# Kernel optimization log

Measured on AMD Instinct MI355X. Metric: run time of the kernel, lower is better.

Reference implementation:

```python
import jax, jax.numpy as jnp
import numpy as np
from jax import lax

B, N = 8, 4096
NPOINT, RADIUS, NSAMPLE = 1024, 0.2, 32
MLP = [64, 64, 128]
FEAT = 64
ALPHA = 0.2          # LeakyReLU slope
BN_EPS = 1e-5        # BatchNorm eps (eval mode, running_mean=0, running_var=1)
BIG = 1e10


def setup_inputs() -> dict:
    key = jax.random.key(0)
    ks = jax.random.split(key, 16)
    xyz = jax.random.uniform(ks[0], (B, N, 3), dtype=jnp.float32)
    feats = jax.random.normal(ks[1], (B, N, FEAT), dtype=jnp.float32)
    d = {"points": jnp.concatenate([xyz, feats], axis=-1)}
    ch = [FEAT] + MLP
    for i in range(len(MLP)):
        d[f"W{i}"] = jax.random.normal(ks[2 + 3 * i], (ch[i + 1], ch[i]), dtype=jnp.float32) * 0.1
        d[f"b{i}"] = jnp.zeros((ch[i + 1],), jnp.float32)
        d[f"g{i}"] = jnp.ones((ch[i + 1],), jnp.float32)
        d[f"be{i}"] = jnp.zeros((ch[i + 1],), jnp.float32)
    d["a_att"] = jax.random.uniform(ks[12], (3 + MLP[-1], MLP[-1]), jnp.float32, -0.3, 0.3)
    return d


def _gather(points, idx):
    # points: [B, N, D], idx: [B, ...] -> [B, ..., D]
    return jax.vmap(lambda p, i: p[i])(points, idx)


def farthest_point_sample(xyz, npoint):
    # xyz: [B, N, 3] -> [B, npoint] (deterministic start at index 0)
    b, n, _ = xyz.shape
    def step(carry, _):
        distance, farthest = carry
        centered = jnp.take_along_axis(xyz, farthest[:, None, None], axis=1)  # [B,1,3]
        dist = jnp.sum((xyz - centered) ** 2, axis=-1)                        # [B,N]
        distance = jnp.minimum(distance, dist)
        return (distance, jnp.argmax(distance, axis=-1)), farthest
    init = (jnp.full((b, n), BIG, dtype=xyz.dtype), jnp.zeros((b,), dtype=jnp.int32))
    _, idxs = lax.scan(step, init, None, length=npoint)
    return jnp.transpose(idxs)  # [B, npoint]


def query_ball_point(nsample, radius, xyz, centered_xyz):
    # squared distances [B, npoint, N]
    d = (-2.0 * jnp.einsum('bpc,bnc->bpn', centered_xyz, xyz)
         + jnp.sum(centered_xyz ** 2, -1)[..., None]
         + jnp.sum(xyz ** 2, -1)[:, None, :])
    d = jnp.where(d > radius ** 2, BIG, d)
    order = jnp.argsort(d, axis=-1)[..., :nsample]                    # [B,np,ns]
    sv = jnp.take_along_axis(d, order, axis=-1)                       # sorted values
    first = order[..., 0:1]
    return jnp.where(sv == BIG, first, order)


def _mlp(x, params):
    # x: [..., C]; 1x1 conv + BN(eval, mean=0, var=1) + relu per layer
    for (W, b, g, be) in params:
        x = jnp.einsum('...c,oc->...o', x, W) + b
        x = x * (g / jnp.sqrt(1.0 + BN_EPS)) + be
        x = jax.nn.relu(x)
    return x


def reference(points, W0, b0, g0, be0, W1, b1, g1, be1, W2, b2, g2, be2, a_att):
    xyz = points[..., :3]
    feats = points[..., 3:]
    cidx = farthest_point_sample(xyz, NPOINT)          # [B, npoint]
    cxyz = _gather(xyz, cidx)                          # [B, npoint, 3]
    cfeat = _gather(feats, cidx)                       # [B, npoint, D]
    gidx = query_ball_point(NSAMPLE, RADIUS, xyz, cxyz)  # [B, npoint, nsample]
    gxyz = _gather(xyz, gidx)                          # [B, npoint, ns, 3]
    gfeat = _gather(feats, gidx)                       # [B, npoint, ns, D]

    params = [(W0, b0, g0, be0), (W1, b1, g1, be1), (W2, b2, g2, be2)]
    cfeat = _mlp(cfeat, params)                        # [B, npoint, D']
    gfeat = _mlp(gfeat, params)                        # [B, npoint, ns, D']

    cpts = jnp.concatenate([cxyz, cfeat], axis=-1)     # [B, npoint, 3+D']
    gpts = jnp.concatenate([gxyz, gfeat], axis=-1)     # [B, npoint, ns, 3+D']

    delta = gpts - cpts[:, :, None, :]
    att = jax.nn.leaky_relu(jnp.einsum('bpnc,cd->bpnd', delta, a_att), ALPHA)
    att = jax.nn.softmax(att, axis=2)                  # over nsample (eval: no dropout)
    gac = jnp.sum(att * gfeat, axis=2)                 # [B, npoint, D']
    return jnp.concatenate([cxyz, gac], axis=-1)       # [B, npoint, 3+D']
```

## Files before the change

### kernel.cpp

```cpp
#include <hip/hip_runtime.h>
#include <math.h>

#define NBATCH 8
#define NPTS 4096
#define NPOINT 1024
#define NSAMPLE 32
#define PTDIM 67
#define BIGF 1e10f

#define DPP_QUAD_XOR1 0xB1
#define DPP_QUAD_XOR2 0x4E
#define DPP_ROW_HALF_MIRROR 0x141
#define DPP_ROW_MIRROR 0x140
#define DPP_ROW_BCAST15 0x142
#define DPP_ROW_BCAST31 0x143

template <int CTRL>
__device__ inline float dpp_mov_f(float v) {
  int i = __float_as_int(v);
  return __int_as_float(__builtin_amdgcn_update_dpp(i, i, CTRL, 0xf, 0xf, false));
}
template <int CTRL>
__device__ inline unsigned dpp_mov_u(unsigned v) {
  return (unsigned)__builtin_amdgcn_update_dpp((int)v, (int)v, CTRL, 0xf, 0xf, false);
}
template <int CTRL>
__device__ inline void dpp_min2(unsigned& hi, unsigned& lo) {
  unsigned nh = dpp_mov_u<CTRL>(hi);
  unsigned nl = dpp_mov_u<CTRL>(lo);
  bool take = (nh < hi) || (nh == hi && nl < lo);
  hi = take ? nh : hi;
  lo = take ? nl : lo;
}
__device__ inline unsigned fmap(float d) {
  unsigned b = __float_as_uint(d);
  return ((int)b < 0) ? ~b : (b | 0x80000000u);
}
#define FMAP_INF 0xFF800000u

__device__ inline float red32_max(float v) {
  v = fmaxf(v, dpp_mov_f<DPP_QUAD_XOR1>(v));
  v = fmaxf(v, dpp_mov_f<DPP_QUAD_XOR2>(v));
  v = fmaxf(v, dpp_mov_f<DPP_ROW_HALF_MIRROR>(v));
  v = fmaxf(v, dpp_mov_f<DPP_ROW_MIRROR>(v));
  v = fmaxf(v, __shfl_xor(v, 16));
  return v;
}
__device__ inline float red32_sum(float v) {
  v += dpp_mov_f<DPP_QUAD_XOR1>(v);
  v += dpp_mov_f<DPP_QUAD_XOR2>(v);
  v += dpp_mov_f<DPP_ROW_HALF_MIRROR>(v);
  v += dpp_mov_f<DPP_ROW_MIRROR>(v);
  v += __shfl_xor(v, 16);
  return v;
}

struct FpsS {
  unsigned long long slots[2][4];
  int cidxS[NPOINT];
  float4 C[NPTS];
};
struct ProjS {
  float As[131 * 128];
  float w0[64 * 64], w1[64 * 64], w2[128 * 64];
  float bb0[64], ss0[64], ee0[64];
  float bb1[64], ss1[64], ee1[64];
  float bb2[128], ss2[128], ee2[128];
};
#define F1_SMEM (sizeof(ProjS) > sizeof(FpsS) ? sizeof(ProjS) : sizeof(FpsS))

__device__ void fps_body(char* smemRaw, const float* __restrict__ pts,
                         int* __restrict__ cidx, float* __restrict__ X,
                         float* __restrict__ Y, float* __restrict__ Z) {
#pragma clang fp contract(off)
  FpsS* S = (FpsS*)smemRaw;
  const int b = blockIdx.x, tid = threadIdx.x;
  const int w = tid >> 6, lane = tid & 63;
  const float* pb = pts + (size_t)b * NPTS * PTDIM;
  float2 px2[8], py2[8], pz2[8];
  float dl[16];
  #pragma unroll
  for (int k = 0; k < 16; k++) {
    int j = tid + (k << 8);
    const float* pj = pb + (size_t)j * PTDIM;
    float x = pj[0], y = pj[1], z = pj[2];
    if (k & 1) { px2[k >> 1].y = x; py2[k >> 1].y = y; pz2[k >> 1].y = z; }
    else       { px2[k >> 1].x = x; py2[k >> 1].x = y; pz2[k >> 1].x = z; }
    S->C[j] = make_float4(x, y, z, 0.0f);
    X[b * NPTS + j] = x; Y[b * NPTS + j] = y; Z[b * NPTS + j] = z;
    dl[k] = BIGF;
  }
  __syncthreads();
  int f = 0;
  float4 c0 = S->C[0];
  float cx = c0.x, cy = c0.y, cz = c0.z;
  for (int t = 0; t < NPOINT; t++) {
    if (tid == 0) S->cidxS[t] = f;
    float2 c2x = make_float2(cx, cx);
    float2 c2y = make_float2(cy, cy);
    float2 c2z = make_float2(cz, cz);
    #pragma unroll
    for (int m = 0; m < 8; m++) {
      float2 dx = px2[m] - c2x;
      float2 dy = py2[m] - c2y;
      float2 dz = pz2[m] - c2z;
      float2 d = (dx * dx + dy * dy) + dz * dz;
      dl[2 * m]     = fminf(dl[2 * m],     d.x);
      dl[2 * m + 1] = fminf(dl[2 * m + 1], d.y);
    }
    float u0 = fmaxf(dl[0], dl[1]),  u1 = fmaxf(dl[2], dl[3]);
    float u2 = fmaxf(dl[4], dl[5]),  u3 = fmaxf(dl[6], dl[7]);
    float u4 = fmaxf(dl[8], dl[9]),  u5 = fmaxf(dl[10], dl[11]);
    float u6 = fmaxf(dl[12], dl[13]), u7 = fmaxf(dl[14], dl[15]);
    float v0 = fmaxf(u0, u1), v1 = fmaxf(u2, u3);
    float v2 = fmaxf(u4, u5), v3 = fmaxf(u6, u7);
    float bv = fmaxf(fmaxf(v0, v1), fmaxf(v2, v3));
    float m = bv;
    m = fmaxf(m, dpp_mov_f<DPP_QUAD_XOR1>(m));
    m = fmaxf(m, dpp_mov_f<DPP_QUAD_XOR2>(m));
    m = fmaxf(m, dpp_mov_f<DPP_ROW_HALF_MIRROR>(m));
    m = fmaxf(m, dpp_mov_f<DPP_ROW_MIRROR>(m));
    m = fmaxf(m, dpp_mov_f<DPP_ROW_BCAST15>(m));
    m = fmaxf(m, dpp_mov_f<DPP_ROW_BCAST31>(m));
    unsigned wmaxbits = (unsigned)__builtin_amdgcn_readlane(__float_as_int(m), 63);
    unsigned c_[16];
    #pragma unroll
    for (int k = 0; k < 16; k++)
      c_[k] = (__float_as_uint(dl[k]) == wmaxbits) ? (unsigned)(tid + (k << 8)) : 0xFFFFFFFFu;
    unsigned q0 = min(c_[0], c_[1]),  q1 = min(c_[2], c_[3]);
    unsigned q2 = min(c_[4], c_[5]),  q3 = min(c_[6], c_[7]);
    unsigned q4 = min(c_[8], c_[9]),  q5 = min(c_[10], c_[11]);
    unsigned q6 = min(c_[12], c_[13]), q7 = min(c_[14], c_[15]);
    unsigned r0 = min(q0, q1), r1 = min(q2, q3), r2 = min(q4, q5), r3 = min(q6, q7);
    unsigned cand = min(min(r0, r1), min(r2, r3));
    cand = min(cand, dpp_mov_u<DPP_QUAD_XOR1>(cand));
    cand = min(cand, dpp_mov_u<DPP_QUAD_XOR2>(cand));
    cand = min(cand, dpp_mov_u<DPP_ROW_HALF_MIRROR>(cand));
    cand = min(cand, dpp_mov_u<DPP_ROW_MIRROR>(cand));
    cand = min(cand, dpp_mov_u<DPP_ROW_BCAST15>(cand));
    cand = min(cand, dpp_mov_u<DPP_ROW_BCAST31>(cand));
    unsigned jmin = (unsigned)__builtin_amdgcn_readlane((int)cand, 63);
    if (lane == 0)
      S->slots[t & 1][w] = ((unsigned long long)wmaxbits << 32) |
                           (unsigned long long)(NPTS - 1 - jmin);
    __syncthreads();
    unsigned long long s0 = S->slots[t & 1][0], s1 = S->slots[t & 1][1];
    unsigned long long s2 = S->slots[t & 1][2], s3 = S->slots[t & 1][3];
    unsigned long long m0 = s0 > s1 ? s0 : s1;
    unsigned long long m1 = s2 > s3 ? s2 : s3;
    unsigned long long best = m0 > m1 ? m0 : m1;
    f = NPTS - 1 - (int)(best & 0xFFFFFFFFull);
    float4 cc = S->C[f];
    cx = cc.x; cy = cc.y; cz = cc.z;
  }
  __syncthreads();
  for (int i = tid; i < NPOINT; i += 256) cidx[b * NPOINT + i] = S->cidxS[i];
}

__device__ void projmlp_body(char* smemRaw, const float* __restrict__ pts,
    const float* __restrict__ W0, const float* __restrict__ B0, const float* __restrict__ G0, const float* __restrict__ E0,
    const float* __restrict__ W1, const float* __restrict__ B1, const float* __restrict__ G1, const float* __restrict__ E1,
    const float* __restrict__ W2, const float* __restrict__ B2, const float* __restrict__ G2, const float* __restrict__ E2,
    const float* __restrict__ Aatt,
    float* __restrict__ mfeat, float* __restrict__ P) {
  ProjS* S = (ProjS*)smemRaw;
  const float INVS = 0.99999500003750f;
  const int t = threadIdx.x;
  for (int i = t; i < 131 * 128; i += 256) S->As[i] = Aatt[i];
  for (int i = t; i < 4096; i += 256) { S->w0[i] = W0[i]; S->w1[i] = W1[i]; }
  for (int i = t; i < 8192; i += 256) S->w2[i] = W2[i];
  if (t < 64) {
    S->bb0[t] = B0[t]; S->ss0[t] = G0[t] * INVS; S->ee0[t] = E0[t];
    S->bb1[t] = B1[t]; S->ss1[t] = G1[t] * INVS; S->ee1[t] = E1[t];
  }
  if (t < 128) { S->bb2[t] = B2[t]; S->ss2[t] = G2[t] * INVS; S->ee2[t] = E2[t]; }
  __syncthreads();

  const int pb = blockIdx.x - 8;
  for (int rr = 0; rr < 2; rr++) {
    const size_t r = (size_t)pb * 512 + rr * 256 + t;
    const float* xr = pts + r * PTDIM + 3;
    float x[64];
    #pragma unroll
    for (int c = 0; c < 64; c++) x[c] = xr[c];

    float h1[64];
    #pragma unroll
    for (int o = 0; o < 64; o++) {
      float acc = S->bb0[o];
      #pragma unroll
      for (int c = 0; c < 64; c += 4) {
        float4 wv = *(const float4*)&S->w0[o * 64 + c];
        acc = fmaf(wv.x, x[c], acc);
        acc = fmaf(wv.y, x[c + 1], acc);
        acc = fmaf(wv.z, x[c + 2], acc);
        acc = fmaf(wv.w, x[c + 3], acc);
      }
      h1[o] = fmaxf(fmaf(acc, S->ss0[o], S->ee0[o]), 0.0f);
    }
    float h2[64];
    #pragma unroll
    for (int o = 0; o < 64; o++) {
      float acc = S->bb1[o];
      #pragma unroll
      for (int c = 0; c < 64; c += 4) {
        float4 wv = *(const float4*)&S->w1[o * 64 + c];
        acc = fmaf(wv.x, h1[c], acc);
        acc = fmaf(wv.y, h1[c + 1], acc);
        acc = fmaf(wv.z, h1[c + 2], acc);
        acc = fmaf(wv.w, h1[c + 3], acc);
      }
      h2[o] = fmaxf(fmaf(acc, S->ss1[o], S->ee1[o]), 0.0f);
    }
    float h3[128];
    float* orow = mfeat + r * 128;
    #pragma unroll
    for (int o = 0; o < 128; o += 4) {
      float a0 = S->bb2[o], a1 = S->bb2[o + 1], a2 = S->bb2[o + 2], a3 = S->bb2[o + 3];
      #pragma unroll
      for (int c = 0; c < 64; c += 4) {
        float4 wv0 = *(const float4*)&S->w2[(o    ) * 64 + c];
        float4 wv1 = *(const float4*)&S->w2[(o + 1) * 64 + c];
        float4 wv2 = *(const float4*)&S->w2[(o + 2) * 64 + c];
        float4 wv3 = *(const float4*)&S->w2[(o + 3) * 64 + c];
        a0 = fmaf(wv0.x, h2[c], a0); a0 = fmaf(wv0.y, h2[c+1], a0); a0 = fmaf(wv0.z, h2[c+2], a0); a0 = fmaf(wv0.w, h2[c+3], a0);
        a1 = fmaf(wv1.x, h2[c], a1); a1 = fmaf(wv1.y, h2[c+1], a1); a1 = fmaf(wv1.z, h2[c+2], a1); a1 = fmaf(wv1.w, h2[c+3], a1);
        a2 = fmaf(wv2.x, h2[c], a2); a2 = fmaf(wv2.y, h2[c+1], a2); a2 = fmaf(wv2.z, h2[c+2], a2); a2 = fmaf(wv2.w, h2[c+3], a2);
        a3 = fmaf(wv3.x, h2[c], a3); a3 = fmaf(wv3.y, h2[c+1], a3); a3 = fmaf(wv3.z, h2[c+2], a3); a3 = fmaf(wv3.w, h2[c+3], a3);
      }
      float4 ov;
      ov.x = fmaxf(fmaf(a0, S->ss2[o    ], S->ee2[o    ]), 0.0f);
      ov.y = fmaxf(fmaf(a1, S->ss2[o + 1], S->ee2[o + 1]), 0.0f);
      ov.z = fmaxf(fmaf(a2, S->ss2[o + 2], S->ee2[o + 2]), 0.0f);
      ov.w = fmaxf(fmaf(a3, S->ss2[o + 3], S->ee2[o + 3]), 0.0f);
      h3[o] = ov.x; h3[o + 1] = ov.y; h3[o + 2] = ov.z; h3[o + 3] = ov.w;
      *(float4*)(orow + o) = ov;
    }
    const float* pr = pts + r * PTDIM;
    float x0 = pr[0], y0 = pr[1], z0 = pr[2];
    float* prow = P + r * 128;
    for (int grp = 0; grp < 4; grp++) {
      const int g0 = grp * 32;
      float acc[32];
      #pragma unroll
      for (int j = 0; j < 32; j++) {
        float a0 = S->As[0 * 128 + g0 + j];
        float a1 = S->As[1 * 128 + g0 + j];
        float a2 = S->As[2 * 128 + g0 + j];
        acc[j] = fmaf(z0, a2, fmaf(y0, a1, x0 * a0));
      }
      #pragma unroll
      for (int c = 0; c < 128; c++) {
        float s = h3[c];
        const float* arow = &S->As[(3 + c) * 128 + g0];
        #pragma unroll
        for (int j = 0; j < 32; j += 4) {
          float4 a = *(const float4*)&arow[j];
          acc[j]   = fmaf(s, a.x, acc[j]);
          acc[j+1] = fmaf(s, a.y, acc[j+1]);
          acc[j+2] = fmaf(s, a.z, acc[j+2]);
          acc[j+3] = fmaf(s, a.w, acc[j+3]);
        }
      }
      #pragma unroll
      for (int j = 0; j < 32; j += 4)
        *(float4*)(prow + g0 + j) = make_float4(acc[j], acc[j+1], acc[j+2], acc[j+3]);
    }
  }
}

__global__ __launch_bounds__(256) void f1_kernel(const float* __restrict__ pts,
    const float* __restrict__ W0, const float* __restrict__ B0, const float* __restrict__ G0, const float* __restrict__ E0,
    const float* __restrict__ W1, const float* __restrict__ B1, const float* __restrict__ G1, const float* __restrict__ E1,
    const float* __restrict__ W2, const float* __restrict__ B2, const float* __restrict__ G2, const float* __restrict__ E2,
    const float* __restrict__ Aatt,
    float* __restrict__ mfeat, float* __restrict__ P, int* __restrict__ cidx,
    float* __restrict__ X, float* __restrict__ Y, float* __restrict__ Z) {
  __shared__ __align__(16) char smem[F1_SMEM];
  if (blockIdx.x < 8)
    fps_body(smem, pts, cidx, X, Y, Z);
  else
    projmlp_body(smem, pts, W0, B0, G0, E0, W1, B1, G1, E1, W2, B2, G2, E2,
                 Aatt, mfeat, P);
}

__global__ __launch_bounds__(256) void f2_kernel(
    const float* __restrict__ X, const float* __restrict__ Y, const float* __restrict__ Z,
    const int* __restrict__ cidx, int* __restrict__ gidx) {
  __shared__ float dbuf[4][512];
  __shared__ int   ibuf[4][512];
  const int t = threadIdx.x;
  const int w = t >> 6, lane = t & 63;
  const int pc = blockIdx.x * 4 + w;
  const int b = pc >> 10;
  const float* Xb = X + b * NPTS;
  const float* Yb = Y + b * NPTS;
  const float* Zb = Z + b * NPTS;
  const int cI = cidx[pc];
  const float cx = Xb[cI], cy = Yb[cI], cz = Zb[cI];
  const float sc = __fadd_rn(__fadd_rn(__fmul_rn(cx, cx), __fmul_rn(cy, cy)), __fmul_rn(cz, cz));
  const float R2 = 0.04f;
  int cnt = 0;
  for (int rr = 0; rr < 16; rr++) {
    const int base = rr * 256 + lane * 4;
    float4 px4 = *(const float4*)(Xb + base);
    float4 py4 = *(const float4*)(Yb + base);
    float4 pz4 = *(const float4*)(Zb + base);
    #pragma unroll
    for (int e = 0; e < 4; e++) {
      float px = e == 0 ? px4.x : e == 1 ? px4.y : e == 2 ? px4.z : px4.w;
      float py = e == 0 ? py4.x : e == 1 ? py4.y : e == 2 ? py4.z : py4.w;
      float pz = e == 0 ? pz4.x : e == 1 ? pz4.y : e == 2 ? pz4.z : pz4.w;
      float dot = __fadd_rn(__fadd_rn(__fmul_rn(cx, px), __fmul_rn(cy, py)), __fmul_rn(cz, pz));
      float sx  = __fadd_rn(__fadd_rn(__fmul_rn(px, px), __fmul_rn(py, py)), __fmul_rn(pz, pz));
      float d   = __fadd_rn(__fadd_rn(__fmul_rn(-2.0f, dot), sc), sx);
      bool pred = !(d > R2);
      unsigned long long mask = __ballot(pred);
      if (pred) {
        int pos = cnt + (int)__popcll(mask & ((1ull << lane) - 1ull));
        if (pos < 512) { dbuf[w][pos] = d; ibuf[w][pos] = base + e; }
      }
      cnt += (int)__popcll(mask);
    }
  }
  const int K = cnt < 512 ? cnt : 512;
  unsigned long long kk[8];
  #pragma unroll
  for (int k = 0; k < 8; k++) {
    int pos = lane + 64 * k;
    if (pos < K)
      kk[k] = ((unsigned long long)fmap(dbuf[w][pos]) << 32) | (unsigned)ibuf[w][pos];
    else
      kk[k] = ((unsigned long long)FMAP_INF << 32) | 0x7fffffffu;
  }
  int first = 0;
  int* gout = gidx + pc * NSAMPLE;
  for (int it = 0; it < NSAMPLE; it++) {
    unsigned long long best = kk[0];
    #pragma unroll
    for (int k = 1; k < 8; k++) if (kk[k] < best) best = kk[k];
    unsigned hi = (unsigned)(best >> 32), lo = (unsigned)best;
    dpp_min2<DPP_QUAD_XOR1>(hi, lo);
    dpp_min2<DPP_QUAD_XOR2>(hi, lo);
    dpp_min2<DPP_ROW_HALF_MIRROR>(hi, lo);
    dpp_min2<DPP_ROW_MIRROR>(hi, lo);
    dpp_min2<DPP_ROW_BCAST15>(hi, lo);
    dpp_min2<DPP_ROW_BCAST31>(hi, lo);
    unsigned blo = (unsigned)__builtin_amdgcn_readlane((int)lo, 63);
    #pragma unroll
    for (int k = 0; k < 8; k++)
      if ((unsigned)kk[k] == blo)
        kk[k] = (kk[k] & 0xFFFFFFFFull) | ((unsigned long long)FMAP_INF << 32);
    if (it == 0) first = (int)blo;
    if (lane == 0) gout[it] = (it < K) ? (int)blo : first;
  }
}

__global__ __launch_bounds__(256) void attn_kernel(
    const float* __restrict__ X, const float* __restrict__ Y, const float* __restrict__ Z,
    const float* __restrict__ mfeat, const float* __restrict__ P,
    const int* __restrict__ cidx, const int* __restrict__ gidx,
    float* __restrict__ out) {
  __shared__ float pcS[128];
  const int pc = (blockIdx.x & 7) * 1024 + (blockIdx.x >> 3);
  const int b = pc >> 10;
  const int t = threadIdx.x;
  const int n = t & 31, q = t >> 5;
  const int cI = cidx[pc];
  if (t < 128) pcS[t] = P[((size_t)b * NPTS + cI) * 128 + t];
  const int g = gidx[pc * NSAMPLE + n];
  const float* Pg = P + ((size_t)b * NPTS + g) * 128 + q * 16;
  const float* Gf = mfeat + ((size_t)b * NPTS + g) * 128 + q * 16;
  __syncthreads();
  float a[16], gfv[16];
  #pragma unroll
  for (int k = 0; k < 4; k++) {
    float4 vg = *(const float4*)(Pg + 4 * k);
    float4 vc = *(const float4*)&pcS[q * 16 + 4 * k];
    float4 vf = *(const float4*)(Gf + 4 * k);
    a[4*k]   = vg.x - vc.x; a[4*k+1] = vg.y - vc.y;
    a[4*k+2] = vg.z - vc.z; a[4*k+3] = vg.w - vc.w;
    gfv[4*k] = vf.x; gfv[4*k+1] = vf.y; gfv[4*k+2] = vf.z; gfv[4*k+3] = vf.w;
  }
  #pragma unroll
  for (int j = 0; j < 16; j++) a[j] = a[j] >= 0.0f ? a[j] : 0.2f * a[j];
  float e[16], s[16], num[16];
  #pragma unroll
  for (int j = 0; j < 16; j++) {
    float mx = red32_max(a[j]);
    e[j] = expf(a[j] - mx);
  }
  #pragma unroll
  for (int j = 0; j < 16; j++) s[j] = red32_sum(e[j]);
  #pragma unroll
  for (int j = 0; j < 16; j++) num[j] = red32_sum(e[j] * gfv[j]);
  if (n == 0) {
    float* orow = out + (size_t)pc * 131;
    #pragma unroll
    for (int j = 0; j < 16; j++) orow[3 + q * 16 + j] = num[j] / s[j];
    if (q == 0) {
      orow[0] = X[b * NPTS + cI]; orow[1] = Y[b * NPTS + cI]; orow[2] = Z[b * NPTS + cI];
    }
  }
}

extern "C" void kernel_launch(void* const* d_in, const int* in_sizes, int n_in,
                              void* d_out, int out_size, void* d_ws, size_t ws_size,
                              hipStream_t stream) {
  const float* points = (const float*)d_in[0];
  const float* W0 = (const float*)d_in[1];
  const float* B0 = (const float*)d_in[2];
  const float* G0 = (const float*)d_in[3];
  const float* E0 = (const float*)d_in[4];
  const float* W1 = (const float*)d_in[5];
  const float* B1 = (const float*)d_in[6];
  const float* G1 = (const float*)d_in[7];
  const float* E1 = (const float*)d_in[8];
  const float* W2 = (const float*)d_in[9];
  const float* B2 = (const float*)d_in[10];
  const float* G2 = (const float*)d_in[11];
  const float* E2 = (const float*)d_in[12];
  const float* Aatt = (const float*)d_in[13];
  float* out = (float*)d_out;

  float* mfeat = (float*)d_ws;
  float* Pw = mfeat + (size_t)NBATCH * NPTS * 128;
  float* Xw = Pw + (size_t)NBATCH * NPTS * 128;
  float* Yw = Xw + NBATCH * NPTS;
  float* Zw = Yw + NBATCH * NPTS;
  int* cidxw = (int*)(Zw + NBATCH * NPTS);
  int* gidxw = cidxw + NBATCH * NPOINT;

  f1_kernel<<<8 + 64, 256, 0, stream>>>(points,
      W0, B0, G0, E0, W1, B1, G1, E1, W2, B2, G2, E2, Aatt,
      mfeat, Pw, cidxw, Xw, Yw, Zw);
  f2_kernel<<<NBATCH * NPOINT / 4, 256, 0, stream>>>(Xw, Yw, Zw, cidxw, gidxw);
  attn_kernel<<<NBATCH * NPOINT, 256, 0, stream>>>(Xw, Yw, Zw, mfeat, Pw, cidxw, gidxw, out);
}
```

Measured before the change: 835.1 us.

## Carry winner coordinates through FPS argmax reduction instead of LDS lookup

The farthest-point-sampling loop now runs a single fused argmax reduction that carries the winning point's index and xyz coordinates through the in-register, DPP and cross-wave stages. This replaces the two-pass scheme (max value, then min index) and drops the shared-memory coordinate table and its dependent load after each barrier. It also skips the unused final distance update. The cost is more DPP moves and selects per reduction step (five values instead of one), in exchange for a shorter serial dependency chain per iteration.

```diff
diff --git a/kernel.cpp b/kernel.cpp
--- a/kernel.cpp
+++ b/kernel.cpp
@@ -55,10 +55,25 @@
   return v;
 }
 
+template <int CTRL>
+__device__ inline void dpp_amax(unsigned& hi, unsigned& lo,
+                                float& x, float& y, float& z) {
+  unsigned nh = dpp_mov_u<CTRL>(hi);
+  unsigned nl = dpp_mov_u<CTRL>(lo);
+  float nx = dpp_mov_f<CTRL>(x);
+  float ny = dpp_mov_f<CTRL>(y);
+  float nz = dpp_mov_f<CTRL>(z);
+  unsigned long long k  = ((unsigned long long)hi << 32) | lo;
+  unsigned long long nk = ((unsigned long long)nh << 32) | nl;
+  bool take = nk > k;
+  hi = take ? nh : hi; lo = take ? nl : lo;
+  x  = take ? nx : x;  y  = take ? ny : y;  z = take ? nz : z;
+}
+
 struct FpsS {
-  unsigned long long slots[2][4];
+  uint4 slotA[2][4];
+  float slotZ[2][4];
   int cidxS[NPOINT];
-  float4 C[NPTS];
 };
 struct ProjS {
   float As[131 * 128];
@@ -86,16 +101,15 @@
     float x = pj[0], y = pj[1], z = pj[2];
     if (k & 1) { px2[k >> 1].y = x; py2[k >> 1].y = y; pz2[k >> 1].y = z; }
     else       { px2[k >> 1].x = x; py2[k >> 1].x = y; pz2[k >> 1].x = z; }
-    S->C[j] = make_float4(x, y, z, 0.0f);
     X[b * NPTS + j] = x; Y[b * NPTS + j] = y; Z[b * NPTS + j] = z;
     dl[k] = BIGF;
   }
-  __syncthreads();
+  const unsigned jb = 4095u - (unsigned)tid;
   int f = 0;
-  float4 c0 = S->C[0];
-  float cx = c0.x, cy = c0.y, cz = c0.z;
+  float cx = pb[0], cy = pb[1], cz = pb[2];
   for (int t = 0; t < NPOINT; t++) {
     if (tid == 0) S->cidxS[t] = f;
+    if (t == NPOINT - 1) break;
     float2 c2x = make_float2(cx, cx);
     float2 c2y = make_float2(cy, cy);
     float2 c2z = make_float2(cz, cz);
@@ -108,50 +122,89 @@
       dl[2 * m]     = fminf(dl[2 * m],     d.x);
       dl[2 * m + 1] = fminf(dl[2 * m + 1], d.y);
     }
-    float u0 = fmaxf(dl[0], dl[1]),  u1 = fmaxf(dl[2], dl[3]);
-    float u2 = fmaxf(dl[4], dl[5]),  u3 = fmaxf(dl[6], dl[7]);
-    float u4 = fmaxf(dl[8], dl[9]),  u5 = fmaxf(dl[10], dl[11]);
-    float u6 = fmaxf(dl[12], dl[13]), u7 = fmaxf(dl[14], dl[15]);
-    float v0 = fmaxf(u0, u1), v1 = fmaxf(u2, u3);
-    float v2 = fmaxf(u4, u5), v3 = fmaxf(u6, u7);
-    float bv = fmaxf(fmaxf(v0, v1), fmaxf(v2, v3));
-    float m = bv;
-    m = fmaxf(m, dpp_mov_f<DPP_QUAD_XOR1>(m));
-    m = fmaxf(m, dpp_mov_f<DPP_QUAD_XOR2>(m));
-    m = fmaxf(m, dpp_mov_f<DPP_ROW_HALF_MIRROR>(m));
-    m = fmaxf(m, dpp_mov_f<DPP_ROW_MIRROR>(m));
-    m = fmaxf(m, dpp_mov_f<DPP_ROW_BCAST15>(m));
-    m = fmaxf(m, dpp_mov_f<DPP_ROW_BCAST31>(m));
-    unsigned wmaxbits = (unsigned)__builtin_amdgcn_readlane(__float_as_int(m), 63);
-    unsigned c_[16];
-    #pragma unroll
-    for (int k = 0; k < 16; k++)
-      c_[k] = (__float_as_uint(dl[k]) == wmaxbits) ? (unsigned)(tid + (k << 8)) : 0xFFFFFFFFu;
-    unsigned q0 = min(c_[0], c_[1]),  q1 = min(c_[2], c_[3]);
-    unsigned q2 = min(c_[4], c_[5]),  q3 = min(c_[6], c_[7]);
-    unsigned q4 = min(c_[8], c_[9]),  q5 = min(c_[10], c_[11]);
-    unsigned q6 = min(c_[12], c_[13]), q7 = min(c_[14], c_[15]);
-    unsigned r0 = min(q0, q1), r1 = min(q2, q3), r2 = min(q4, q5), r3 = min(q6, q7);
-    unsigned cand = min(min(r0, r1), min(r2, r3));
-    cand = min(cand, dpp_mov_u<DPP_QUAD_XOR1>(cand));
-    cand = min(cand, dpp_mov_u<DPP_QUAD_XOR2>(cand));
-    cand = min(cand, dpp_mov_u<DPP_ROW_HALF_MIRROR>(cand));
-    cand = min(cand, dpp_mov_u<DPP_ROW_MIRROR>(cand));
-    cand = min(cand, dpp_mov_u<DPP_ROW_BCAST15>(cand));
-    cand = min(cand, dpp_mov_u<DPP_ROW_BCAST31>(cand));
-    unsigned jmin = (unsigned)__builtin_amdgcn_readlane((int)cand, 63);
-    if (lane == 0)
-      S->slots[t & 1][w] = ((unsigned long long)wmaxbits << 32) |
-                           (unsigned long long)(NPTS - 1 - jmin);
+    float td[8]; unsigned tj[8]; float tx[8], ty[8], tz[8];
+    #pragma unroll
+    for (int m = 0; m < 8; m++) {
+      bool take = dl[2 * m + 1] > dl[2 * m];
+      td[m] = take ? dl[2 * m + 1] : dl[2 * m];
+      tj[m] = jb - (unsigned)((take ? (2 * m + 1) : (2 * m)) << 8);
+      tx[m] = take ? px2[m].y : px2[m].x;
+      ty[m] = take ? py2[m].y : py2[m].x;
+      tz[m] = take ? pz2[m].y : pz2[m].x;
+    }
+    #pragma unroll
+    for (int m = 0; m < 4; m++) {
+      bool take = td[2 * m + 1] > td[2 * m];
+      td[m] = take ? td[2 * m + 1] : td[2 * m];
+      tj[m] = take ? tj[2 * m + 1] : tj[2 * m];
+      tx[m] = take ? tx[2 * m + 1] : tx[2 * m];
+      ty[m] = take ? ty[2 * m + 1] : ty[2 * m];
+      tz[m] = take ? tz[2 * m + 1] : tz[2 * m];
+    }
+    #pragma unroll
+    for (int m = 0; m < 2; m++) {
+      bool take = td[2 * m + 1] > td[2 * m];
+      td[m] = take ? td[2 * m + 1] : td[2 * m];
+      tj[m] = take ? tj[2 * m + 1] : tj[2 * m];
+      tx[m] = take ? tx[2 * m + 1] : tx[2 * m];
+      ty[m] = take ? ty[2 * m + 1] : ty[2 * m];
+      tz[m] = take ? tz[2 * m + 1] : tz[2 * m];
+    }
+    {
+      bool take = td[1] > td[0];
+      td[0] = take ? td[1] : td[0];
+      tj[0] = take ? tj[1] : tj[0];
+      tx[0] = take ? tx[1] : tx[0];
+      ty[0] = take ? ty[1] : ty[0];
+      tz[0] = take ? tz[1] : tz[0];
+    }
+    unsigned bhi = __float_as_uint(td[0]);
+    unsigned bjp = tj[0];
+    float bx = tx[0], by = ty[0], bz = tz[0];
+    dpp_amax<DPP_QUAD_XOR1>(bhi, bjp, bx, by, bz);
+    dpp_amax<DPP_QUAD_XOR2>(bhi, bjp, bx, by, bz);
+    dpp_amax<DPP_ROW_HALF_MIRROR>(bhi, bjp, bx, by, bz);
+    dpp_amax<DPP_ROW_MIRROR>(bhi, bjp, bx, by, bz);
+    dpp_amax<DPP_ROW_BCAST15>(bhi, bjp, bx, by, bz);
+    dpp_amax<DPP_ROW_BCAST31>(bhi, bjp, bx, by, bz);
+    if (lane == 63) {
+      S->slotA[t & 1][w] = make_uint4(bhi, bjp, __float_as_uint(bx),
+                                      __float_as_uint(by));
+      S->slotZ[t & 1][w] = bz;
+    }
     __syncthreads();
-    unsigned long long s0 = S->slots[t & 1][0], s1 = S->slots[t & 1][1];
-    unsigned long long s2 = S->slots[t & 1][2], s3 = S->slots[t & 1][3];
-    unsigned long long m0 = s0 > s1 ? s0 : s1;
-    unsigned long long m1 = s2 > s3 ? s2 : s3;
-    unsigned long long best = m0 > m1 ? m0 : m1;
-    f = NPTS - 1 - (int)(best & 0xFFFFFFFFull);
-    float4 cc = S->C[f];
-    cx = cc.x; cy = cc.y; cz = cc.z;
+    uint4 q0 = S->slotA[t & 1][0]; float z0 = S->slotZ[t & 1][0];
+    uint4 q1 = S->slotA[t & 1][1]; float z1 = S->slotZ[t & 1][1];
+    uint4 q2 = S->slotA[t & 1][2]; float z2 = S->slotZ[t & 1][2];
+    uint4 q3 = S->slotA[t & 1][3]; float z3 = S->slotZ[t & 1][3];
+    {
+      unsigned long long k0 = ((unsigned long long)q0.x << 32) | q0.y;
+      unsigned long long k1 = ((unsigned long long)q1.x << 32) | q1.y;
+      bool take = k1 > k0;
+      q0.x = take ? q1.x : q0.x; q0.y = take ? q1.y : q0.y;
+      q0.z = take ? q1.z : q0.z; q0.w = take ? q1.w : q0.w;
+      z0   = take ? z1 : z0;
+    }
+    {
+      unsigned long long k2 = ((unsigned long long)q2.x << 32) | q2.y;
+      unsigned long long k3 = ((unsigned long long)q3.x << 32) | q3.y;
+      bool take = k3 > k2;
+      q2.x = take ? q3.x : q2.x; q2.y = take ? q3.y : q2.y;
+      q2.z = take ? q3.z : q2.z; q2.w = take ? q3.w : q2.w;
+      z2   = take ? z3 : z2;
+    }
+    {
+      unsigned long long k0 = ((unsigned long long)q0.x << 32) | q0.y;
+      unsigned long long k2 = ((unsigned long long)q2.x << 32) | q2.y;
+      bool take = k2 > k0;
+      q0.y = take ? q2.y : q0.y;
+      q0.z = take ? q2.z : q0.z; q0.w = take ? q2.w : q0.w;
+      z0   = take ? z2 : z0;
+    }
+    f = (int)(4095u - q0.y);
+    cx = __uint_as_float(q0.z);
+    cy = __uint_as_float(q0.w);
+    cz = z0;
   }
   __syncthreads();
   for (int i = tid; i < NPOINT; i += 256) cidx[b * NPOINT + i] = S->cidxS[i];
```

New measurement: 1.235 ms. +47.9%, slower.

## Fuse FPS, ball query and attention into one persistent producer-consumer kernel

Applied to the files above, without the earlier changes.

Merges the three launches into one kernel. FPS blocks publish each centroid index to global memory with an atomic store as soon as it is picked. Consumer blocks spin on those flags and immediately run the ball query and the attention softmax for each centroid, waiting on a per-batch done counter before reading the MLP projections. The goal is to hide the neighbour search and attention work behind the long serial FPS loop and to drop the gidx round trip and extra launches. In exchange it relies on every block being resident at the same time, on spin-waits with a capped retry count, and on only 128 consumer blocks handling all of the attention work.

```diff
diff --git a/kernel.cpp b/kernel.cpp
--- a/kernel.cpp
+++ b/kernel.cpp
@@ -7,6 +7,8 @@
 #define NSAMPLE 32
 #define PTDIM 67
 #define BIGF 1e10f
+#define NCONS 128
+#define SPIN_CAP 4096
 
 #define DPP_QUAD_XOR1 0xB1
 #define DPP_QUAD_XOR2 0x4E
@@ -57,7 +59,6 @@
 
 struct FpsS {
   unsigned long long slots[2][4];
-  int cidxS[NPOINT];
   float4 C[NPTS];
 };
 struct ProjS {
@@ -67,7 +68,15 @@
   float bb1[64], ss1[64], ee1[64];
   float bb2[128], ss2[128], ee2[128];
 };
-#define F1_SMEM (sizeof(ProjS) > sizeof(FpsS) ? sizeof(ProjS) : sizeof(FpsS))
+struct ConsS {
+  float dbuf[4][512];
+  int   ibuf[4][512];
+  int   gidxS[4][32];
+  int   cIS[4];
+  float pcS[128];
+};
+#define SMX1 (sizeof(ProjS) > sizeof(FpsS) ? sizeof(ProjS) : sizeof(FpsS))
+#define F1_SMEM (SMX1 > sizeof(ConsS) ? SMX1 : sizeof(ConsS))
 
 __device__ void fps_body(char* smemRaw, const float* __restrict__ pts,
                          int* __restrict__ cidx, float* __restrict__ X,
@@ -90,12 +99,15 @@
     X[b * NPTS + j] = x; Y[b * NPTS + j] = y; Z[b * NPTS + j] = z;
     dl[k] = BIGF;
   }
+  __threadfence();
   __syncthreads();
   int f = 0;
   float4 c0 = S->C[0];
   float cx = c0.x, cy = c0.y, cz = c0.z;
   for (int t = 0; t < NPOINT; t++) {
-    if (tid == 0) S->cidxS[t] = f;
+    if (tid == 0)
+      __hip_atomic_store(&cidx[b * NPOINT + t], f, __ATOMIC_RELAXED,
+                         __HIP_MEMORY_SCOPE_AGENT);
     float2 c2x = make_float2(cx, cx);
     float2 c2y = make_float2(cy, cy);
     float2 c2z = make_float2(cz, cz);
@@ -153,8 +165,6 @@
     float4 cc = S->C[f];
     cx = cc.x; cy = cc.y; cz = cc.z;
   }
-  __syncthreads();
-  for (int i = tid; i < NPOINT; i += 256) cidx[b * NPOINT + i] = S->cidxS[i];
 }
 
 __device__ void projmlp_body(char* smemRaw, const float* __restrict__ pts,
@@ -162,7 +172,7 @@
     const float* __restrict__ W1, const float* __restrict__ B1, const float* __restrict__ G1, const float* __restrict__ E1,
     const float* __restrict__ W2, const float* __restrict__ B2, const float* __restrict__ G2, const float* __restrict__ E2,
     const float* __restrict__ Aatt,
-    float* __restrict__ mfeat, float* __restrict__ P) {
+    float* __restrict__ mfeat, float* __restrict__ P, int* __restrict__ done) {
   ProjS* S = (ProjS*)smemRaw;
   const float INVS = 0.99999500003750f;
   const int t = threadIdx.x;
@@ -267,141 +277,170 @@
         *(float4*)(prow + g0 + j) = make_float4(acc[j], acc[j+1], acc[j+2], acc[j+3]);
     }
   }
-}
-
-__global__ __launch_bounds__(256) void f1_kernel(const float* __restrict__ pts,
+  __threadfence();
+  __syncthreads();
+  if (t == 0)
+    __hip_atomic_fetch_add(&done[pb >> 3], 1, __ATOMIC_RELEASE,
+                           __HIP_MEMORY_SCOPE_AGENT);
+}
+
+__device__ void consumer_body(char* smemRaw,
+    const float* __restrict__ X, const float* __restrict__ Y, const float* __restrict__ Z,
+    const float* __restrict__ mfeat, const float* __restrict__ P,
+    int* __restrict__ cidx, int* __restrict__ done,
+    float* __restrict__ out, int c) {
+  ConsS* S = (ConsS*)smemRaw;
+  const int t = threadIdx.x;
+  const int w = t >> 6, lane = t & 63;
+  const int b = c >> 4, r = c & 15;
+  const float* Xb = X + b * NPTS;
+  const float* Yb = Y + b * NPTS;
+  const float* Zb = Z + b * NPTS;
+  const float R2 = 0.04f;
+
+  for (int i = 0; i < 16; i++) {
+    const int tpos = r + 16 * (4 * i + w);
+    const int pc = b * NPOINT + tpos;
+    for (int spin = 0; spin < SPIN_CAP; ++spin) {
+      if (__hip_atomic_load(&cidx[pc], __ATOMIC_RELAXED,
+                            __HIP_MEMORY_SCOPE_AGENT) != -1) break;
+      __builtin_amdgcn_s_sleep(64);
+    }
+    int cI = __hip_atomic_load(&cidx[pc], __ATOMIC_ACQUIRE,
+                               __HIP_MEMORY_SCOPE_AGENT);
+    if (cI < 0) cI = 0;
+    if (lane == 0) S->cIS[w] = cI;
+    const float cx = Xb[cI], cy = Yb[cI], cz = Zb[cI];
+    const float sc = __fadd_rn(__fadd_rn(__fmul_rn(cx, cx), __fmul_rn(cy, cy)), __fmul_rn(cz, cz));
+    int cnt = 0;
+    for (int rr = 0; rr < 16; rr++) {
+      const int base = rr * 256 + lane * 4;
+      float4 px4 = *(const float4*)(Xb + base);
+      float4 py4 = *(const float4*)(Yb + base);
+      float4 pz4 = *(const float4*)(Zb + base);
+      #pragma unroll
+      for (int e = 0; e < 4; e++) {
+        float px = e == 0 ? px4.x : e == 1 ? px4.y : e == 2 ? px4.z : px4.w;
+        float py = e == 0 ? py4.x : e == 1 ? py4.y : e == 2 ? py4.z : py4.w;
+        float pz = e == 0 ? pz4.x : e == 1 ? pz4.y : e == 2 ? pz4.z : pz4.w;
+        float dot = __fadd_rn(__fadd_rn(__fmul_rn(cx, px), __fmul_rn(cy, py)), __fmul_rn(cz, pz));
+        float sx  = __fadd_rn(__fadd_rn(__fmul_rn(px, px), __fmul_rn(py, py)), __fmul_rn(pz, pz));
+        float d   = __fadd_rn(__fadd_rn(__fmul_rn(-2.0f, dot), sc), sx);
+        bool pred = !(d > R2);
+        unsigned long long mask = __ballot(pred);
+        if (pred) {
+          int pos = cnt + (int)__popcll(mask & ((1ull << lane) - 1ull));
+          if (pos < 512) { S->dbuf[w][pos] = d; S->ibuf[w][pos] = base + e; }
+        }
+        cnt += (int)__popcll(mask);
+      }
+    }
+    const int K = cnt < 512 ? cnt : 512;
+    unsigned long long kk[8];
+    #pragma unroll
+    for (int kq = 0; kq < 8; kq++) {
+      int pos = lane + 64 * kq;
+      if (pos < K)
+        kk[kq] = ((unsigned long long)fmap(S->dbuf[w][pos]) << 32) | (unsigned)S->ibuf[w][pos];
+      else
+        kk[kq] = ((unsigned long long)FMAP_INF << 32) | 0x7fffffffu;
+    }
+    int first = 0;
+    for (int it = 0; it < NSAMPLE; it++) {
+      unsigned long long best = kk[0];
+      #pragma unroll
+      for (int kq = 1; kq < 8; kq++) if (kk[kq] < best) best = kk[kq];
+      unsigned hi = (unsigned)(best >> 32), lo = (unsigned)best;
+      dpp_min2<DPP_QUAD_XOR1>(hi, lo);
+      dpp_min2<DPP_QUAD_XOR2>(hi, lo);
+      dpp_min2<DPP_ROW_HALF_MIRROR>(hi, lo);
+      dpp_min2<DPP_ROW_MIRROR>(hi, lo);
+      dpp_min2<DPP_ROW_BCAST15>(hi, lo);
+      dpp_min2<DPP_ROW_BCAST31>(hi, lo);
+      unsigned blo = (unsigned)__builtin_amdgcn_readlane((int)lo, 63);
+      #pragma unroll
+      for (int kq = 0; kq < 8; kq++)
+        if ((unsigned)kk[kq] == blo)
+          kk[kq] = (kk[kq] & 0xFFFFFFFFull) | ((unsigned long long)FMAP_INF << 32);
+      if (it == 0) first = (int)blo;
+      if (lane == 0) S->gidxS[w][it] = (it < K) ? (int)blo : first;
+    }
+    __syncthreads();
+    if (i == 0) {
+      for (int spin = 0; spin < SPIN_CAP; ++spin) {
+        if (__hip_atomic_load(&done[b], __ATOMIC_ACQUIRE,
+                              __HIP_MEMORY_SCOPE_AGENT) >= 8) break;
+        __builtin_amdgcn_s_sleep(64);
+      }
+    }
+    for (int cc = 0; cc < 4; cc++) {
+      const int pcc = b * NPOINT + r + 16 * (4 * i + cc);
+      const int cIc = S->cIS[cc];
+      if (t < 128) S->pcS[t] = P[((size_t)b * NPTS + cIc) * 128 + t];
+      __syncthreads();
+      const int n = t & 31, q = t >> 5;
+      const int g = S->gidxS[cc][n];
+      const float* Pg = P + ((size_t)b * NPTS + g) * 128 + q * 16;
+      const float* Gf = mfeat + ((size_t)b * NPTS + g) * 128 + q * 16;
+      float a[16], gfv[16];
+      #pragma unroll
+      for (int kq = 0; kq < 4; kq++) {
+        float4 vg = *(const float4*)(Pg + 4 * kq);
+        float4 vc = *(const float4*)&S->pcS[q * 16 + 4 * kq];
+        float4 vf = *(const float4*)(Gf + 4 * kq);
+        a[4*kq]   = vg.x - vc.x; a[4*kq+1] = vg.y - vc.y;
+        a[4*kq+2] = vg.z - vc.z; a[4*kq+3] = vg.w - vc.w;
+        gfv[4*kq] = vf.x; gfv[4*kq+1] = vf.y; gfv[4*kq+2] = vf.z; gfv[4*kq+3] = vf.w;
+      }
+      #pragma unroll
+      for (int j = 0; j < 16; j++) a[j] = a[j] >= 0.0f ? a[j] : 0.2f * a[j];
+      float e[16], s[16], num[16];
+      #pragma unroll
+      for (int j = 0; j < 16; j++) {
+        float mx = red32_max(a[j]);
+        e[j] = expf(a[j] - mx);
+      }
+      #pragma unroll
+      for (int j = 0; j < 16; j++) s[j] = red32_sum(e[j]);
+      #pragma unroll
+      for (int j = 0; j < 16; j++) num[j] = red32_sum(e[j] * gfv[j]);
+      if (n == 0) {
+        float* orow = out + (size_t)pcc * 131;
+        #pragma unroll
+        for (int j = 0; j < 16; j++) orow[3 + q * 16 + j] = num[j] / s[j];
+        if (q == 0) {
+          orow[0] = Xb[cIc]; orow[1] = Yb[cIc]; orow[2] = Zb[cIc];
+        }
+      }
+      __syncthreads();
+    }
+  }
+}
+
+__global__ __launch_bounds__(256) void mega_kernel(const float* __restrict__ pts,
     const float* __restrict__ W0, const float* __restrict__ B0, const float* __restrict__ G0, const float* __restrict__ E0,
     const float* __restrict__ W1, const float* __restrict__ B1, const float* __restrict__ G1, const float* __restrict__ E1,
     const float* __restrict__ W2, const float* __restrict__ B2, const float* __restrict__ G2, const float* __restrict__ E2,
     const float* __restrict__ Aatt,
     float* __restrict__ mfeat, float* __restrict__ P, int* __restrict__ cidx,
-    float* __restrict__ X, float* __restrict__ Y, float* __restrict__ Z) {
+    int* __restrict__ done,
+    float* __restrict__ X, float* __restrict__ Y, float* __restrict__ Z,
+    float* __restrict__ out) {
   __shared__ __align__(16) char smem[F1_SMEM];
   if (blockIdx.x < 8)
     fps_body(smem, pts, cidx, X, Y, Z);
+  else if (blockIdx.x < 72)
+    projmlp_body(smem, pts, W0, B0, G0, E0, W1, B1, G1, E1, W2, B2, G2, E2,
+                 Aatt, mfeat, P, done);
   else
-    projmlp_body(smem, pts, W0, B0, G0, E0, W1, B1, G1, E1, W2, B2, G2, E2,
-                 Aatt, mfeat, P);
-}
-
-__global__ __launch_bounds__(256) void f2_kernel(
-    const float* __restrict__ X, const float* __restrict__ Y, const float* __restrict__ Z,
-    const int* __restrict__ cidx, int* __restrict__ gidx) {
-  __shared__ float dbuf[4][512];
-  __shared__ int   ibuf[4][512];
-  const int t = threadIdx.x;
-  const int w = t >> 6, lane = t & 63;
-  const int pc = blockIdx.x * 4 + w;
-  const int b = pc >> 10;
-  const float* Xb = X + b * NPTS;
-  const float* Yb = Y + b * NPTS;
-  const float* Zb = Z + b * NPTS;
-  const int cI = cidx[pc];
-  const float cx = Xb[cI], cy = Yb[cI], cz = Zb[cI];
-  const float sc = __fadd_rn(__fadd_rn(__fmul_rn(cx, cx), __fmul_rn(cy, cy)), __fmul_rn(cz, cz));
-  const float R2 = 0.04f;
-  int cnt = 0;
-  for (int rr = 0; rr < 16; rr++) {
-    const int base = rr * 256 + lane * 4;
-    float4 px4 = *(const float4*)(Xb + base);
-    float4 py4 = *(const float4*)(Yb + base);
-    float4 pz4 = *(const float4*)(Zb + base);
-    #pragma unroll
-    for (int e = 0; e < 4; e++) {
-      float px = e == 0 ? px4.x : e == 1 ? px4.y : e == 2 ? px4.z : px4.w;
-      float py = e == 0 ? py4.x : e == 1 ? py4.y : e == 2 ? py4.z : py4.w;
-      float pz = e == 0 ? pz4.x : e == 1 ? pz4.y : e == 2 ? pz4.z : pz4.w;
-      float dot = __fadd_rn(__fadd_rn(__fmul_rn(cx, px), __fmul_rn(cy, py)), __fmul_rn(cz, pz));
-      float sx  = __fadd_rn(__fadd_rn(__fmul_rn(px, px), __fmul_rn(py, py)), __fmul_rn(pz, pz));
-      float d   = __fadd_rn(__fadd_rn(__fmul_rn(-2.0f, dot), sc), sx);
-      bool pred = !(d > R2);
-      unsigned long long mask = __ballot(pred);
-      if (pred) {
-        int pos = cnt + (int)__popcll(mask & ((1ull << lane) - 1ull));
-        if (pos < 512) { dbuf[w][pos] = d; ibuf[w][pos] = base + e; }
-      }
-      cnt += (int)__popcll(mask);
-    }
-  }
-  const int K = cnt < 512 ? cnt : 512;
-  unsigned long long kk[8];
-  #pragma unroll
-  for (int k = 0; k < 8; k++) {
-    int pos = lane + 64 * k;
-    if (pos < K)
-      kk[k] = ((unsigned long long)fmap(dbuf[w][pos]) << 32) | (unsigned)ibuf[w][pos];
-    else
-      kk[k] = ((unsigned long long)FMAP_INF << 32) | 0x7fffffffu;
-  }
-  int first = 0;
-  int* gout = gidx + pc * NSAMPLE;
-  for (int it = 0; it < NSAMPLE; it++) {
-    unsigned long long best = kk[0];
-    #pragma unroll
-    for (int k = 1; k < 8; k++) if (kk[k] < best) best = kk[k];
-    unsigned hi = (unsigned)(best >> 32), lo = (unsigned)best;
-    dpp_min2<DPP_QUAD_XOR1>(hi, lo);
-    dpp_min2<DPP_QUAD_XOR2>(hi, lo);
-    dpp_min2<DPP_ROW_HALF_MIRROR>(hi, lo);
-    dpp_min2<DPP_ROW_MIRROR>(hi, lo);
-    dpp_min2<DPP_ROW_BCAST15>(hi, lo);
-    dpp_min2<DPP_ROW_BCAST31>(hi, lo);
-    unsigned blo = (unsigned)__builtin_amdgcn_readlane((int)lo, 63);
-    #pragma unroll
-    for (int k = 0; k < 8; k++)
-      if ((unsigned)kk[k] == blo)
-        kk[k] = (kk[k] & 0xFFFFFFFFull) | ((unsigned long long)FMAP_INF << 32);
-    if (it == 0) first = (int)blo;
-    if (lane == 0) gout[it] = (it < K) ? (int)blo : first;
-  }
-}
-
-__global__ __launch_bounds__(256) void attn_kernel(
-    const float* __restrict__ X, const float* __restrict__ Y, const float* __restrict__ Z,
-    const float* __restrict__ mfeat, const float* __restrict__ P,
-    const int* __restrict__ cidx, const int* __restrict__ gidx,
-    float* __restrict__ out) {
-  __shared__ float pcS[128];
-  const int pc = (blockIdx.x & 7) * 1024 + (blockIdx.x >> 3);
-  const int b = pc >> 10;
-  const int t = threadIdx.x;
-  const int n = t & 31, q = t >> 5;
-  const int cI = cidx[pc];
-  if (t < 128) pcS[t] = P[((size_t)b * NPTS + cI) * 128 + t];
-  const int g = gidx[pc * NSAMPLE + n];
-  const float* Pg = P + ((size_t)b * NPTS + g) * 128 + q * 16;
-  const float* Gf = mfeat + ((size_t)b * NPTS + g) * 128 + q * 16;
-  __syncthreads();
-  float a[16], gfv[16];
-  #pragma unroll
-  for (int k = 0; k < 4; k++) {
-    float4 vg = *(const float4*)(Pg + 4 * k);
-    float4 vc = *(const float4*)&pcS[q * 16 + 4 * k];
-    float4 vf = *(const float4*)(Gf + 4 * k);
-    a[4*k]   = vg.x - vc.x; a[4*k+1] = vg.y - vc.y;
-    a[4*k+2] = vg.z - vc.z; a[4*k+3] = vg.w - vc.w;
-    gfv[4*k] = vf.x; gfv[4*k+1] = vf.y; gfv[4*k+2] = vf.z; gfv[4*k+3] = vf.w;
-  }
-  #pragma unroll
-  for (int j = 0; j < 16; j++) a[j] = a[j] >= 0.0f ? a[j] : 0.2f * a[j];
-  float e[16], s[16], num[16];
-  #pragma unroll
-  for (int j = 0; j < 16; j++) {
-    float mx = red32_max(a[j]);
-    e[j] = expf(a[j] - mx);
-  }
-  #pragma unroll
-  for (int j = 0; j < 16; j++) s[j] = red32_sum(e[j]);
-  #pragma unroll
-  for (int j = 0; j < 16; j++) num[j] = red32_sum(e[j] * gfv[j]);
-  if (n == 0) {
-    float* orow = out + (size_t)pc * 131;
-    #pragma unroll
-    for (int j = 0; j < 16; j++) orow[3 + q * 16 + j] = num[j] / s[j];
-    if (q == 0) {
-      orow[0] = X[b * NPTS + cI]; orow[1] = Y[b * NPTS + cI]; orow[2] = Z[b * NPTS + cI];
-    }
-  }
+    consumer_body(smem, X, Y, Z, mfeat, P, cidx, done, out, blockIdx.x - 72);
+}
+
+__global__ __launch_bounds__(256) void init_kernel(int* __restrict__ cidx,
+                                                   int* __restrict__ done) {
+  int i = blockIdx.x * 256 + threadIdx.x;
+  if (i < NBATCH * NPOINT) cidx[i] = -1;
+  if (i < NBATCH) done[i] = 0;
 }
 
 extern "C" void kernel_launch(void* const* d_in, const int* in_sizes, int n_in,
@@ -429,11 +468,10 @@
   float* Yw = Xw + NBATCH * NPTS;
   float* Zw = Yw + NBATCH * NPTS;
   int* cidxw = (int*)(Zw + NBATCH * NPTS);
-  int* gidxw = cidxw + NBATCH * NPOINT;
-
-  f1_kernel<<<8 + 64, 256, 0, stream>>>(points,
+  int* donew = cidxw + NBATCH * NPOINT;
+
+  init_kernel<<<32, 256, 0, stream>>>(cidxw, donew);
+  mega_kernel<<<8 + 64 + NCONS, 256, 0, stream>>>(points,
       W0, B0, G0, E0, W1, B1, G1, E1, W2, B2, G2, E2, Aatt,
-      mfeat, Pw, cidxw, Xw, Yw, Zw);
-  f2_kernel<<<NBATCH * NPOINT / 4, 256, 0, stream>>>(Xw, Yw, Zw, cidxw, gidxw);
-  attn_kernel<<<NBATCH * NPOINT, 256, 0, stream>>>(Xw, Yw, Zw, mfeat, Pw, cidxw, gidxw, out);
-}
+      mfeat, Pw, cidxw, donew, Xw, Yw, Zw, out);
+}
```

Measured after the change: 1.332 ms. +59.5%, slower.
